# Optimization experiments

Measured on AMD Instinct MI355X. Metric: run time of the kernel, lower is better.

The kernel has to match this reference:

```python
import jax, jax.numpy as jnp
import numpy as np

B, L, H = 32, 256, 384
MAX_WAVE = 2048  # config.max_wave_length


def setup_inputs() -> dict:
    key = jax.random.key(0)
    k1, k2 = jax.random.split(key)
    encoder_hidden_states = jax.random.normal(k1, (B, L, H), dtype=jnp.float32)
    durations_gt = jax.random.randint(k2, (B, L), 0, 15, dtype=jnp.int32)
    return {"encoder_hidden_states": encoder_hidden_states, "durations_gt": durations_gt}


def reference(encoder_hidden_states, durations_gt):
    # Length regulation: token i is repeated durations_gt[b, i] times along the
    # output frame axis; frames past the total length are zero-padded.
    csum = jnp.cumsum(durations_gt, axis=1)               # [B, L] inclusive cumsum
    total = csum[:, -1]                                    # [B] real lengths
    t = jnp.arange(MAX_WAVE, dtype=csum.dtype)             # [T]
    # frame t belongs to token idx where csum[idx-1] <= t < csum[idx]
    idx = jax.vmap(lambda c: jnp.searchsorted(c, t, side="right"))(csum)  # [B, T]
    valid = t[None, :] < total[:, None]                    # [B, T]
    safe_idx = jnp.clip(idx, 0, L - 1)
    gathered = jnp.take_along_axis(encoder_hidden_states, safe_idx[..., None], axis=1)  # [B, T, H]
    gathered = jnp.where(valid[..., None], gathered, 0.0)
    outputs = jnp.transpose(gathered, (0, 2, 1))           # [B, H, T] per custom-op output shape
    encoder_masks = valid.astype(encoder_hidden_states.dtype)  # [B, T]
    return outputs, encoder_masks
```

## Files before the change

kernel.cpp:

```cpp
#include <hip/hip_runtime.h>

constexpr int Lc = 256;
constexpr int Hc = 384;
constexpr int Tc = 2048;
constexpr int Bc = 32;
constexpr int H_TILE = 16;
constexpr int PADW = 20;

typedef float floatx4 __attribute__((ext_vector_type(4)));

__global__ __launch_bounds__(512) void lr_fused_kernel(
    const float* __restrict__ enc,
    const int*   __restrict__ dur,
    float*       __restrict__ out,
    float*       __restrict__ mask)
{
    const int tid  = threadIdx.x;
    const int lane = tid & 63;
    const int wv   = tid >> 6;
    const int b    = blockIdx.y;
    const int h0   = blockIdx.x * H_TILE;

    __shared__ float          s_enc[Lc * PADW];
    __shared__ unsigned short s_row[Tc];
    __shared__ int            s_wtot[8];

    const float* encb = enc + (size_t)b * (Lc * Hc) + h0;
    const int r  = tid >> 2;
    const int c4 = (tid & 3) * 4;
    floatx4 st[2];
#pragma unroll
    for (int p = 0; p < 2; ++p)
        st[p] = *reinterpret_cast<const floatx4*>(encb + (size_t)(r + p * 128) * Hc + c4);

    int d = 0;
    if (tid < Lc) d = dur[b * Lc + tid];
    {
        uint2 f; f.x = 0x00FF00FFu; f.y = 0x00FF00FFu;
        *reinterpret_cast<uint2*>(s_row + tid * 4) = f;
    }

    int s = d;
#pragma unroll
    for (int off = 1; off < 64; off <<= 1) {
        int t = __shfl_up(s, off);
        if (lane >= off) s += t;
    }
    if (lane == 63) s_wtot[wv] = s;

#pragma unroll
    for (int p = 0; p < 2; ++p) {
        float* dst = s_enc + (r + p * 128) * PADW + c4;
        dst[0] = st[p].x; dst[1] = st[p].y; dst[2] = st[p].z; dst[3] = st[p].w;
    }

    __syncthreads();

    int pre = 0, total = 0;
#pragma unroll
    for (int w = 0; w < 4; ++w) {
        int t = s_wtot[w];
        total += t;
        if (w < wv) pre += t;
    }
    if (tid < Lc) {
        const int csum_i = s + pre;
        const int excl   = csum_i - d;
        int hiw = csum_i; if (hiw > Tc) hiw = Tc;
        for (int t = excl; t < hiw; ++t) s_row[t] = (unsigned short)tid;
    }

    __syncthreads();

    const int tbase = tid * 4;
    ushort4 iv = *reinterpret_cast<const ushort4*>(s_row + tbase);

    const int rowoff0 = (int)iv.x * PADW;
    const int rowoff1 = (int)iv.y * PADW;
    const int rowoff2 = (int)iv.z * PADW;
    const int rowoff3 = (int)iv.w * PADW;
    const float m0 = (tbase + 0 < total) ? 1.0f : 0.0f;
    const float m1 = (tbase + 1 < total) ? 1.0f : 0.0f;
    const float m2 = (tbase + 2 < total) ? 1.0f : 0.0f;
    const float m3 = (tbase + 3 < total) ? 1.0f : 0.0f;

    float* outb = out + (size_t)b * (Hc * Tc) + (size_t)h0 * Tc + tbase;
#pragma unroll
    for (int hh0 = 0; hh0 < H_TILE; hh0 += 4) {
        floatx4 a0 = *reinterpret_cast<const floatx4*>(s_enc + rowoff0 + hh0);
        floatx4 a1 = *reinterpret_cast<const floatx4*>(s_enc + rowoff1 + hh0);
        floatx4 a2 = *reinterpret_cast<const floatx4*>(s_enc + rowoff2 + hh0);
        floatx4 a3 = *reinterpret_cast<const floatx4*>(s_enc + rowoff3 + hh0);
#pragma unroll
        for (int j = 0; j < 4; ++j) {
            floatx4 v;
            v.x = a0[j] * m0;
            v.y = a1[j] * m1;
            v.z = a2[j] * m2;
            v.w = a3[j] * m3;
            __builtin_nontemporal_store(
                v, reinterpret_cast<floatx4*>(outb + (size_t)(hh0 + j) * Tc));
        }
    }

    if (blockIdx.x == 0) {
        floatx4 m; m.x = m0; m.y = m1; m.z = m2; m.w = m3;
        __builtin_nontemporal_store(
            m, reinterpret_cast<floatx4*>(mask + (size_t)b * Tc + tbase));
    }
}

extern "C" void kernel_launch(void* const* d_in, const int* in_sizes, int n_in,
                              void* d_out, int out_size, void* d_ws, size_t ws_size,
                              hipStream_t stream) {
    const float* enc = (const float*)d_in[0];
    const int*   dur = (const int*)d_in[1];

    float* out  = (float*)d_out;
    float* mask = out + (size_t)Bc * Hc * Tc;

    dim3 grid(Hc / H_TILE, Bc);
    dim3 block(512);
    lr_fused_kernel<<<grid, block, 0, stream>>>(enc, dur, out, mask);
}
```

Measured before the change: 24.11 us.

## Process three H tiles per block with double-buffered LDS prefetch

Each block now handles three consecutive 16-wide H tiles (8 groups per batch) instead of one. This cuts the grid from 768 to 256 blocks and amortises the per-block duration scan and index-map construction across three tiles. The next tile's encoder slice is loaded into registers while the current tile is written out, then stored into a second LDS buffer. The trade-off is fewer blocks for the 256 CUs, so only one block per CU, and less parallelism to hide store latency.

```diff
diff --git a/kernel.cpp b/kernel.cpp
--- a/kernel.cpp
+++ b/kernel.cpp
@@ -5,7 +5,8 @@
 constexpr int Tc = 2048;
 constexpr int Bc = 32;
 constexpr int H_TILE = 16;
-constexpr int PADW = 20;
+constexpr int NTILE  = 3;
+constexpr int PADW   = 20;
 
 typedef float floatx4 __attribute__((ext_vector_type(4)));
 
@@ -18,20 +19,23 @@
     const int tid  = threadIdx.x;
     const int lane = tid & 63;
     const int wv   = tid >> 6;
-    const int b    = blockIdx.y;
-    const int h0   = blockIdx.x * H_TILE;
+    const int b    = blockIdx.x >> 3;
+    const int hg   = blockIdx.x & 7;
 
-    __shared__ float          s_enc[Lc * PADW];
-    __shared__ unsigned short s_row[Tc];
-    __shared__ int            s_wtot[8];
+    __shared__ alignas(16) float          s_enc[2][Lc * PADW];
+    __shared__ alignas(16) unsigned short s_row[Tc];
+    __shared__ int s_wtot[8];
 
-    const float* encb = enc + (size_t)b * (Lc * Hc) + h0;
+    const float* encb = enc + (size_t)b * (Lc * Hc);
     const int r  = tid >> 2;
     const int c4 = (tid & 3) * 4;
+
     floatx4 st[2];
-#pragma unroll
-    for (int p = 0; p < 2; ++p)
-        st[p] = *reinterpret_cast<const floatx4*>(encb + (size_t)(r + p * 128) * Hc + c4);
+    {
+        const float* p0 = encb + hg * (NTILE * H_TILE) + c4;
+        st[0] = *reinterpret_cast<const floatx4*>(p0 + (size_t)r * Hc);
+        st[1] = *reinterpret_cast<const floatx4*>(p0 + (size_t)(r + 128) * Hc);
+    }
 
     int d = 0;
     if (tid < Lc) d = dur[b * Lc + tid];
@@ -48,10 +52,10 @@
     }
     if (lane == 63) s_wtot[wv] = s;
 
-#pragma unroll
-    for (int p = 0; p < 2; ++p) {
-        float* dst = s_enc + (r + p * 128) * PADW + c4;
-        dst[0] = st[p].x; dst[1] = st[p].y; dst[2] = st[p].z; dst[3] = st[p].w;
+    {
+        float* dst = &s_enc[0][r * PADW + c4];
+        *reinterpret_cast<floatx4*>(dst) = st[0];
+        *reinterpret_cast<floatx4*>(&s_enc[0][(r + 128) * PADW + c4]) = st[1];
     }
 
     __syncthreads();
@@ -74,39 +78,58 @@
 
     const int tbase = tid * 4;
     ushort4 iv = *reinterpret_cast<const ushort4*>(s_row + tbase);
-
-    const int rowoff0 = (int)iv.x * PADW;
-    const int rowoff1 = (int)iv.y * PADW;
-    const int rowoff2 = (int)iv.z * PADW;
-    const int rowoff3 = (int)iv.w * PADW;
+    const int ro0 = (int)iv.x * PADW;
+    const int ro1 = (int)iv.y * PADW;
+    const int ro2 = (int)iv.z * PADW;
+    const int ro3 = (int)iv.w * PADW;
     const float m0 = (tbase + 0 < total) ? 1.0f : 0.0f;
     const float m1 = (tbase + 1 < total) ? 1.0f : 0.0f;
     const float m2 = (tbase + 2 < total) ? 1.0f : 0.0f;
     const float m3 = (tbase + 3 < total) ? 1.0f : 0.0f;
 
-    float* outb = out + (size_t)b * (Hc * Tc) + (size_t)h0 * Tc + tbase;
-#pragma unroll
-    for (int hh0 = 0; hh0 < H_TILE; hh0 += 4) {
-        floatx4 a0 = *reinterpret_cast<const floatx4*>(s_enc + rowoff0 + hh0);
-        floatx4 a1 = *reinterpret_cast<const floatx4*>(s_enc + rowoff1 + hh0);
-        floatx4 a2 = *reinterpret_cast<const floatx4*>(s_enc + rowoff2 + hh0);
-        floatx4 a3 = *reinterpret_cast<const floatx4*>(s_enc + rowoff3 + hh0);
-#pragma unroll
-        for (int j = 0; j < 4; ++j) {
-            floatx4 v;
-            v.x = a0[j] * m0;
-            v.y = a1[j] * m1;
-            v.z = a2[j] * m2;
-            v.w = a3[j] * m3;
-            __builtin_nontemporal_store(
-                v, reinterpret_cast<floatx4*>(outb + (size_t)(hh0 + j) * Tc));
-        }
-    }
-
-    if (blockIdx.x == 0) {
+    if (hg == 0) {
         floatx4 m; m.x = m0; m.y = m1; m.z = m2; m.w = m3;
         __builtin_nontemporal_store(
             m, reinterpret_cast<floatx4*>(mask + (size_t)b * Tc + tbase));
+    }
+
+    float* outB = out + (size_t)b * (Hc * Tc) + tbase;
+#pragma unroll
+    for (int k = 0; k < NTILE; ++k) {
+        const int cur = k & 1;
+
+        if (k + 1 < NTILE) {
+            const float* pn = encb + hg * (NTILE * H_TILE) + (k + 1) * H_TILE + c4;
+            st[0] = *reinterpret_cast<const floatx4*>(pn + (size_t)r * Hc);
+            st[1] = *reinterpret_cast<const floatx4*>(pn + (size_t)(r + 128) * Hc);
+        }
+
+        const float* sb = s_enc[cur];
+        float* outb = outB + (size_t)((hg * NTILE + k) * H_TILE) * Tc;
+#pragma unroll
+        for (int hh0 = 0; hh0 < H_TILE; hh0 += 4) {
+            floatx4 a0 = *reinterpret_cast<const floatx4*>(sb + ro0 + hh0);
+            floatx4 a1 = *reinterpret_cast<const floatx4*>(sb + ro1 + hh0);
+            floatx4 a2 = *reinterpret_cast<const floatx4*>(sb + ro2 + hh0);
+            floatx4 a3 = *reinterpret_cast<const floatx4*>(sb + ro3 + hh0);
+#pragma unroll
+            for (int j = 0; j < 4; ++j) {
+                floatx4 v;
+                v.x = a0[j] * m0;
+                v.y = a1[j] * m1;
+                v.z = a2[j] * m2;
+                v.w = a3[j] * m3;
+                __builtin_nontemporal_store(
+                    v, reinterpret_cast<floatx4*>(outb + (size_t)(hh0 + j) * Tc));
+            }
+        }
+
+        if (k + 1 < NTILE) {
+            float* dstb = const_cast<float*>(s_enc[cur ^ 1]);
+            *reinterpret_cast<floatx4*>(dstb + r * PADW + c4) = st[0];
+            *reinterpret_cast<floatx4*>(dstb + (r + 128) * PADW + c4) = st[1];
+            __syncthreads();
+        }
     }
 }
 
@@ -119,7 +142,7 @@
     float* out  = (float*)d_out;
     float* mask = out + (size_t)Bc * Hc * Tc;
 
-    dim3 grid(Hc / H_TILE, Bc);
+    dim3 grid(Bc * 8);
     dim3 block(512);
     lr_fused_kernel<<<grid, block, 0, stream>>>(enc, dur, out, mask);
 }
```

Result: slower. 26.30 us (+9.1%).
